# Kernel tuning notes

Measured on AMD Instinct MI355X. Metric: run time of the kernel, lower is better.

The kernel has to match this reference:

```python
import jax, jax.numpy as jnp
import numpy as np

THRESHOLD = 0.25
W_CD, W_FID, W_NC, W_SYM, W_DIFF = 1.0, 0.5, 0.1, 0.1, 1.0
KL_BETA = 0.0  # _step = 0 at init -> kl_beta = beta_max * min(1, 0/5000) = 0


def _cdist(p1, p2):
    # torch.cdist(p=2): [B,N,3] x [B,M,3] -> [B,N,M]
    sq1 = jnp.sum(p1 * p1, axis=-1)  # [B,N]
    sq2 = jnp.sum(p2 * p2, axis=-1)  # [B,M]
    d2 = sq1[:, :, None] + sq2[:, None, :] - 2.0 * jnp.einsum('bnd,bmd->bnm', p1, p2)
    return jnp.sqrt(jnp.maximum(d2, 0.0))


def _chamfer_l1(p1, p2):
    dist = _cdist(p1, p2)
    cd = dist.min(axis=2).mean(axis=1) + dist.min(axis=1).mean(axis=1)
    return cd.mean()


def setup_inputs() -> dict:
    key = jax.random.key(0)
    ks = jax.random.split(key, 11)
    B, N, M, P, D = 4, 4096, 4096, 2048, 512
    pn = jax.random.normal(ks[7], (B, 3), dtype=jnp.float32)
    pn = pn / jnp.linalg.norm(pn, axis=-1, keepdims=True)  # unit plane normals
    return {
        'pred': jax.random.normal(ks[0], (B, N, 3), dtype=jnp.float32),
        'full': jax.random.normal(ks[1], (B, M, 3), dtype=jnp.float32),
        'partial': jax.random.normal(ks[2], (B, P, 3), dtype=jnp.float32),
        'mu': jax.random.normal(ks[3], (B, D), dtype=jnp.float32),
        'logvar': jax.random.normal(ks[4], (B, D), dtype=jnp.float32),
        'pred_normals': jax.random.normal(ks[5], (B, N, 3), dtype=jnp.float32),
        'gt_normals': jax.random.normal(ks[6], (B, N, 3), dtype=jnp.float32),
        'plane_normals': pn,
        'plane_offsets': jax.random.normal(ks[8], (B,), dtype=jnp.float32) * 0.1,
        'sym_confidences': jax.random.uniform(ks[9], (B,), dtype=jnp.float32),
        'diffusion_loss': jax.random.uniform(ks[10], (), dtype=jnp.float32),
    }


def reference(pred, full, partial, mu, logvar, pred_normals, gt_normals,
              plane_normals, plane_offsets, sym_confidences, diffusion_loss):
    # chamfer L1
    cd = _chamfer_l1(pred, full)
    # KL divergence of diagonal Gaussian
    kl = (-0.5 * (1.0 + logvar - mu * mu - jnp.exp(logvar))).sum(axis=-1).mean()
    # fidelity: partial -> pred nearest-neighbor distance
    fid = _cdist(partial, pred).min(axis=2).mean()
    # normal consistency: 1 - |cos|
    num = jnp.sum(pred_normals * gt_normals, axis=-1)
    den = jnp.linalg.norm(pred_normals, axis=-1) * jnp.linalg.norm(gt_normals, axis=-1)
    cos = num / jnp.maximum(den, 1e-8)
    nc = (1.0 - jnp.abs(cos)).mean()
    # bilateral symmetry error (confidence-gated), vectorized over batch
    off = jax.lax.stop_gradient(plane_offsets)  # torch uses .item() -> constant
    s = jnp.einsum('bnd,bd->bn', pred, plane_normals) + off[:, None]  # signed dist
    reflected = pred - 2.0 * s[..., None] * plane_normals[:, None, :]
    dist = _cdist(pred, reflected)
    cd_l1_b = dist.min(axis=2).mean(axis=1) + dist.min(axis=1).mean(axis=1)  # [B]
    sym_b = jnp.where(sym_confidences >= THRESHOLD,
                      sym_confidences * cd_l1_b * 0.5, 0.0)
    sym = sym_b.mean()
    total = (W_CD * cd + KL_BETA * kl + W_FID * fid + W_NC * nc
             + W_SYM * sym + W_DIFF * diffusion_loss)
    return total
```

## Files before the change

kernel.cpp:

```cpp
#include <hip/hip_runtime.h>

#define BB 4
#define NN 4096
#define MM 4096
#define PP 2048

#define TILE 512
#define NTILE 8
#define SPLIT 64
#define QPT 16
#define QPB 64


__global__ __launch_bounds__(256, 4) void fused_kernel(
    const float* __restrict__ pred, const float* __restrict__ full,
    const float* __restrict__ partial, const float* __restrict__ plane_n,
    const float* __restrict__ plane_off,
    const float* __restrict__ pn, const float* __restrict__ gn,
    float* __restrict__ ws)
{
    int blk = blockIdx.x;
    int tid = threadIdx.x;
    __shared__ float4 sc[2][TILE];
    __shared__ float sred[4];

    if (blk >= 896) {
        int i = (blk - 896) * 256 + tid;
        const float* p = pn + (size_t)i * 3;
        const float* g = gn + (size_t)i * 3;
        float px = p[0], py = p[1], pz = p[2];
        float gx = g[0], gy = g[1], gz = g[2];
        float num = fmaf(px, gx, fmaf(py, gy, pz * gz));
        float den = sqrtf(fmaf(px, px, fmaf(py, py, pz * pz))) *
                    sqrtf(fmaf(gx, gx, fmaf(gy, gy, gz * gz)));
        float v = 1.f - fabsf(num / fmaxf(den, 1e-8f));
        for (int o = 1; o < 64; o <<= 1) v += __shfl_xor(v, o);
        if ((tid & 63) == 0) sred[tid >> 6] = v;
        __syncthreads();
        if (tid == 0) ws[blk] = sred[0] + sred[1] + sred[2] + sred[3];
        return;
    }

    const float* qptr; const float* cptr; int b, qbase;
    bool reflect = false;
    if (blk < 256) {
        b = blk >> 6; qbase = (blk & 63) * QPB;
        qptr = pred + b * NN * 3; cptr = full + b * MM * 3;
    } else if (blk < 512) {
        int t = blk - 256; b = t >> 6; qbase = (t & 63) * QPB;
        qptr = full + b * MM * 3; cptr = pred + b * NN * 3;
    } else if (blk < 640) {
        int t = blk - 512; b = t >> 5; qbase = (t & 31) * QPB;
        qptr = partial + b * PP * 3; cptr = pred + b * NN * 3;
    } else {
        int t = blk - 640; b = t >> 6; qbase = (t & 63) * QPB;
        qptr = pred + b * NN * 3; cptr = pred + b * NN * 3;
        reflect = true;
    }

    int lane = tid & 63;
    int wv = tid >> 6;

    float nx = 0.f, ny = 0.f, nz = 0.f, noff = 0.f;
    if (reflect) {
        nx = plane_n[b * 3 + 0]; ny = plane_n[b * 3 + 1]; nz = plane_n[b * 3 + 2];
        noff = plane_off[b];
    }

    float ax[QPT], ay[QPT], az[QPT], q2[QPT], md[QPT];
#pragma unroll
    for (int j = 0; j < QPT; ++j) {
        int qi = qbase + wv * QPT + j;
        float x = qptr[qi * 3 + 0];
        float y = qptr[qi * 3 + 1];
        float z = qptr[qi * 3 + 2];
        q2[j] = fmaf(x, x, fmaf(y, y, z * z));
        ax[j] = -2.f * x; ay[j] = -2.f * y; az[j] = -2.f * z;
        md[j] = 3.4e38f;
    }

    float c0x, c0y, c0z, c1x, c1y, c1z;

#define LOADT(TB) do { \
        const float* cp0 = cptr + (size_t)((TB) + tid) * 3; \
        c0x = cp0[0]; c0y = cp0[1]; c0z = cp0[2]; \
        const float* cp1 = cptr + (size_t)((TB) + tid + 256) * 3; \
        c1x = cp1[0]; c1y = cp1[1]; c1z = cp1[2]; \
    } while (0)

#define WRITET(BUF) do { \
        float x = c0x, y = c0y, z = c0z; \
        if (reflect) { \
            float sd = fmaf(x, nx, fmaf(y, ny, fmaf(z, nz, noff))); \
            float t2 = 2.0f * sd; \
            x -= t2 * nx; y -= t2 * ny; z -= t2 * nz; \
        } \
        (BUF)[tid] = make_float4(x, y, z, fmaf(x, x, fmaf(y, y, z * z))); \
        x = c1x; y = c1y; z = c1z; \
        if (reflect) { \
            float sd = fmaf(x, nx, fmaf(y, ny, fmaf(z, nz, noff))); \
            float t2 = 2.0f * sd; \
            x -= t2 * nx; y -= t2 * ny; z -= t2 * nz; \
        } \
        (BUF)[tid + 256] = make_float4(x, y, z, fmaf(x, x, fmaf(y, y, z * z))); \
    } while (0)

    LOADT(0);
    WRITET(sc[0]);
    __syncthreads();

    for (int t = 0; t < NTILE; ++t) {
        int cur = t & 1;
        if (t + 1 < NTILE) LOADT((t + 1) * TILE);
        const float4* scc = sc[cur];
#pragma unroll
        for (int k = 0; k < TILE / SPLIT; ++k) {
            float4 c = scc[lane + k * SPLIT];
#pragma unroll
            for (int j = 0; j < QPT; ++j) {
                float v = fmaf(ax[j], c.x, fmaf(ay[j], c.y, fmaf(az[j], c.z, c.w)));
                md[j] = fminf(md[j], v);
            }
        }
        __syncthreads();
        if (t + 1 < NTILE) WRITET(sc[cur ^ 1]);
        __syncthreads();
    }

#pragma unroll
    for (int j = 0; j < QPT; ++j) {
        md[j] = fminf(md[j], __shfl_xor(md[j], 1));
        md[j] = fminf(md[j], __shfl_xor(md[j], 2));
        md[j] = fminf(md[j], __shfl_xor(md[j], 4));
        md[j] = fminf(md[j], __shfl_xor(md[j], 8));
        md[j] = fminf(md[j], __shfl_xor(md[j], 16));
        md[j] = fminf(md[j], __shfl_xor(md[j], 32));
    }
    if (lane == 0) {
        float part = 0.f;
#pragma unroll
        for (int j = 0; j < QPT; ++j)
            part += sqrtf(fmaxf(q2[j] + md[j], 0.f));
        sred[wv] = part;
    }
    __syncthreads();
    if (tid == 0)
        ws[blk] = sred[0] + sred[1] + sred[2] + sred[3];
}

__global__ __launch_bounds__(256) void final_kernel(
    const float* __restrict__ ws,
    const float* __restrict__ confs,
    const float* __restrict__ diff,
    float* __restrict__ out)
{
    __shared__ float seg[8];
    int tid = threadIdx.x;
    if (tid < 8) seg[tid] = 0.f;
    __syncthreads();
    for (int i = tid; i < 960; i += 256) {
        float v = ws[i];
        int sgi;
        if (i < 256) sgi = 0;
        else if (i < 512) sgi = 1;
        else if (i < 640) sgi = 2;
        else if (i < 896) sgi = 3 + ((i - 640) >> 6);
        else sgi = 7;
        atomicAdd(&seg[sgi], v);
    }
    __syncthreads();
    if (tid == 0) {
        const float BN = (float)(BB * NN);
        const float BM = (float)(BB * MM);
        const float BP = (float)(BB * PP);
        float cd  = seg[0] / BN + seg[1] / BM;
        float fid = seg[2] / BP;
        float nc  = seg[7] / BN;
        float sym = 0.f;
#pragma unroll
        for (int b = 0; b < BB; ++b) {
            float conf = confs[b];
            if (conf >= 0.25f) {
                float cdl1 = 2.0f * seg[3 + b] / (float)NN;
                sym += conf * cdl1 * 0.5f;
            }
        }
        sym *= (1.0f / BB);
        out[0] = 1.0f * cd + 0.5f * fid + 0.1f * nc + 0.1f * sym + diff[0];
    }
}

extern "C" void kernel_launch(void* const* d_in, const int* in_sizes, int n_in,
                              void* d_out, int out_size, void* d_ws, size_t ws_size,
                              hipStream_t stream) {
    const float* pred      = (const float*)d_in[0];
    const float* full      = (const float*)d_in[1];
    const float* partial   = (const float*)d_in[2];
    const float* pred_n    = (const float*)d_in[5];
    const float* gt_n      = (const float*)d_in[6];
    const float* plane_n   = (const float*)d_in[7];
    const float* plane_off = (const float*)d_in[8];
    const float* confs     = (const float*)d_in[9];
    const float* diff      = (const float*)d_in[10];
    float* ws = (float*)d_ws;

    fused_kernel<<<960, 256, 0, stream>>>(pred, full, partial, plane_n,
                                          plane_off, pred_n, gt_n, ws);
    final_kernel<<<1, 256, 0, stream>>>(ws, confs, diff, (float*)d_out);
}
```

Baseline: 37.48 us.

## Keep candidate points in registers and stream queries instead of LDS tiles

The nearest-neighbor kernel is restructured so that each of the two waves holds 32 candidates per lane in registers (covering all 4096 candidates). Queries are streamed in groups of 4 as wave-uniform loads, and the per-wave minima are combined through a small shared array. This removes the double-buffered LDS tiles and their per-tile barriers. In exchange the block size drops to 128 threads with many more registers per thread, which may lower occupancy, and queries are reloaded from global memory. Each candidate is reused for only 4 queries, where the old code reused each LDS load across 16 queries.

```diff
diff --git a/kernel.cpp b/kernel.cpp
--- a/kernel.cpp
+++ b/kernel.cpp
@@ -5,14 +5,12 @@
 #define MM 4096
 #define PP 2048
 
-#define TILE 512
-#define NTILE 8
-#define SPLIT 64
-#define QPT 16
+#define CPL 32
 #define QPB 64
+#define QG 4
 
 
-__global__ __launch_bounds__(256, 4) void fused_kernel(
+__global__ __launch_bounds__(128, 2) void fused_kernel(
     const float* __restrict__ pred, const float* __restrict__ full,
     const float* __restrict__ partial, const float* __restrict__ plane_n,
     const float* __restrict__ plane_off,
@@ -21,11 +19,11 @@
 {
     int blk = blockIdx.x;
     int tid = threadIdx.x;
-    __shared__ float4 sc[2][TILE];
-    __shared__ float sred[4];
+    __shared__ float wmin[2][QPB];
+    __shared__ float sred[2];
 
     if (blk >= 896) {
-        int i = (blk - 896) * 256 + tid;
+        int i = (blk - 896) * 128 + tid;
         const float* p = pn + (size_t)i * 3;
         const float* g = gn + (size_t)i * 3;
         float px = p[0], py = p[1], pz = p[2];
@@ -37,7 +35,7 @@
         for (int o = 1; o < 64; o <<= 1) v += __shfl_xor(v, o);
         if ((tid & 63) == 0) sred[tid >> 6] = v;
         __syncthreads();
-        if (tid == 0) ws[blk] = sred[0] + sred[1] + sred[2] + sred[3];
+        if (tid == 0) ws[blk] = sred[0] + sred[1];
         return;
     }
 
@@ -60,6 +58,7 @@
 
     int lane = tid & 63;
     int wv = tid >> 6;
+    int cbase = wv * (CPL * 64);
 
     float nx = 0.f, ny = 0.f, nz = 0.f, noff = 0.f;
     if (reflect) {
@@ -67,85 +66,67 @@
         noff = plane_off[b];
     }
 
-    float ax[QPT], ay[QPT], az[QPT], q2[QPT], md[QPT];
+    float cxm2[CPL], cym2[CPL], czm2[CPL], c2[CPL];
 #pragma unroll
-    for (int j = 0; j < QPT; ++j) {
-        int qi = qbase + wv * QPT + j;
-        float x = qptr[qi * 3 + 0];
-        float y = qptr[qi * 3 + 1];
-        float z = qptr[qi * 3 + 2];
-        q2[j] = fmaf(x, x, fmaf(y, y, z * z));
-        ax[j] = -2.f * x; ay[j] = -2.f * y; az[j] = -2.f * z;
-        md[j] = 3.4e38f;
+    for (int k = 0; k < CPL; ++k) {
+        const float* cp = cptr + (size_t)(cbase + k * 64 + lane) * 3;
+        float x = cp[0], y = cp[1], z = cp[2];
+        if (reflect) {
+            float sd = fmaf(x, nx, fmaf(y, ny, fmaf(z, nz, noff)));
+            float t2 = 2.0f * sd;
+            x -= t2 * nx; y -= t2 * ny; z -= t2 * nz;
+        }
+        c2[k]   = fmaf(x, x, fmaf(y, y, z * z));
+        cxm2[k] = -2.f * x; cym2[k] = -2.f * y; czm2[k] = -2.f * z;
     }
 
-    float c0x, c0y, c0z, c1x, c1y, c1z;
+    for (int qg = 0; qg < QPB / QG; ++qg) {
+        const float* qp = qptr + (size_t)(qbase + qg * QG) * 3;
+        float qx[QG], qy[QG], qz[QG], mdv[QG];
+#pragma unroll
+        for (int j = 0; j < QG; ++j) {
+            qx[j] = qp[j * 3 + 0];
+            qy[j] = qp[j * 3 + 1];
+            qz[j] = qp[j * 3 + 2];
+            mdv[j] = 3.4e38f;
+        }
+#pragma unroll
+        for (int k = 0; k < CPL; ++k) {
+#pragma unroll
+            for (int j = 0; j < QG; ++j) {
+                float t = fmaf(czm2[k], qz[j], c2[k]);
+                t = fmaf(cym2[k], qy[j], t);
+                t = fmaf(cxm2[k], qx[j], t);
+                mdv[j] = fminf(mdv[j], t);
+            }
+        }
+#pragma unroll
+        for (int j = 0; j < QG; ++j) {
+            mdv[j] = fminf(mdv[j], __shfl_xor(mdv[j], 1));
+            mdv[j] = fminf(mdv[j], __shfl_xor(mdv[j], 2));
+            mdv[j] = fminf(mdv[j], __shfl_xor(mdv[j], 4));
+            mdv[j] = fminf(mdv[j], __shfl_xor(mdv[j], 8));
+            mdv[j] = fminf(mdv[j], __shfl_xor(mdv[j], 16));
+            mdv[j] = fminf(mdv[j], __shfl_xor(mdv[j], 32));
+        }
+        if (lane == 0) {
+#pragma unroll
+            for (int j = 0; j < QG; ++j)
+                wmin[wv][qg * QG + j] = mdv[j];
+        }
+    }
 
-#define LOADT(TB) do { \
-        const float* cp0 = cptr + (size_t)((TB) + tid) * 3; \
-        c0x = cp0[0]; c0y = cp0[1]; c0z = cp0[2]; \
-        const float* cp1 = cptr + (size_t)((TB) + tid + 256) * 3; \
-        c1x = cp1[0]; c1y = cp1[1]; c1z = cp1[2]; \
-    } while (0)
-
-#define WRITET(BUF) do { \
-        float x = c0x, y = c0y, z = c0z; \
-        if (reflect) { \
-            float sd = fmaf(x, nx, fmaf(y, ny, fmaf(z, nz, noff))); \
-            float t2 = 2.0f * sd; \
-            x -= t2 * nx; y -= t2 * ny; z -= t2 * nz; \
-        } \
-        (BUF)[tid] = make_float4(x, y, z, fmaf(x, x, fmaf(y, y, z * z))); \
-        x = c1x; y = c1y; z = c1z; \
-        if (reflect) { \
-            float sd = fmaf(x, nx, fmaf(y, ny, fmaf(z, nz, noff))); \
-            float t2 = 2.0f * sd; \
-            x -= t2 * nx; y -= t2 * ny; z -= t2 * nz; \
-        } \
-        (BUF)[tid + 256] = make_float4(x, y, z, fmaf(x, x, fmaf(y, y, z * z))); \
-    } while (0)
-
-    LOADT(0);
-    WRITET(sc[0]);
     __syncthreads();
 
-    for (int t = 0; t < NTILE; ++t) {
-        int cur = t & 1;
-        if (t + 1 < NTILE) LOADT((t + 1) * TILE);
-        const float4* scc = sc[cur];
-#pragma unroll
-        for (int k = 0; k < TILE / SPLIT; ++k) {
-            float4 c = scc[lane + k * SPLIT];
-#pragma unroll
-            for (int j = 0; j < QPT; ++j) {
-                float v = fmaf(ax[j], c.x, fmaf(ay[j], c.y, fmaf(az[j], c.z, c.w)));
-                md[j] = fminf(md[j], v);
-            }
-        }
-        __syncthreads();
-        if (t + 1 < NTILE) WRITET(sc[cur ^ 1]);
-        __syncthreads();
+    if (tid < QPB) {
+        float m = fminf(wmin[0][tid], wmin[1][tid]);
+        const float* qp = qptr + (size_t)(qbase + tid) * 3;
+        float x = qp[0], y = qp[1], z = qp[2];
+        float q2 = fmaf(x, x, fmaf(y, y, z * z));
+        float d = sqrtf(fmaxf(q2 + m, 0.f));
+        for (int o = 1; o < 64; o <<= 1) d += __shfl_xor(d, o);
+        if (tid == 0) ws[blk] = d;
     }
-
-#pragma unroll
-    for (int j = 0; j < QPT; ++j) {
-        md[j] = fminf(md[j], __shfl_xor(md[j], 1));
-        md[j] = fminf(md[j], __shfl_xor(md[j], 2));
-        md[j] = fminf(md[j], __shfl_xor(md[j], 4));
-        md[j] = fminf(md[j], __shfl_xor(md[j], 8));
-        md[j] = fminf(md[j], __shfl_xor(md[j], 16));
-        md[j] = fminf(md[j], __shfl_xor(md[j], 32));
-    }
-    if (lane == 0) {
-        float part = 0.f;
-#pragma unroll
-        for (int j = 0; j < QPT; ++j)
-            part += sqrtf(fmaxf(q2[j] + md[j], 0.f));
-        sred[wv] = part;
-    }
-    __syncthreads();
-    if (tid == 0)
-        ws[blk] = sred[0] + sred[1] + sred[2] + sred[3];
 }
 
 __global__ __launch_bounds__(256) void final_kernel(
@@ -158,7 +139,7 @@
     int tid = threadIdx.x;
     if (tid < 8) seg[tid] = 0.f;
     __syncthreads();
-    for (int i = tid; i < 960; i += 256) {
+    for (int i = tid; i < 1024; i += 256) {
         float v = ws[i];
         int sgi;
         if (i < 256) sgi = 0;
@@ -204,7 +185,7 @@
     const float* diff      = (const float*)d_in[10];
     float* ws = (float*)d_ws;
 
-    fused_kernel<<<960, 256, 0, stream>>>(pred, full, partial, plane_n,
-                                          plane_off, pred_n, gt_n, ws);
+    fused_kernel<<<1024, 128, 0, stream>>>(pred, full, partial, plane_n,
+                                           plane_off, pred_n, gt_n, ws);
     final_kernel<<<1, 256, 0, stream>>>(ws, confs, diff, (float*)d_out);
 }
```

After: 41.93 us. 1.12x slower.
